# Optimization experiments

Hardware: AMD Instinct MI355X
Metric: run time of the kernel (lower is better)

## Reference

```python
import jax, jax.numpy as jnp
import numpy as np

B = 100000          # polymers
MOLS_PER = 4        # 3 monomers + 1 solvent per polymer
N = B * MOLS_PER
D = 64              # rdkit feature dim
F = 64              # polymer-level feature dim
H = 128             # hidden dim


def setup_inputs() -> dict:
    key = jax.random.key(0)
    ks = jax.random.split(key, 6)
    polymer_feats = jax.random.normal(ks[0], (B, F), dtype=jnp.float32)
    rdkit = jax.random.normal(ks[1], (N, D), dtype=jnp.float32)
    # sorted segment ids; last molecule of each segment is the solvent
    polymer_mapping = jnp.repeat(jnp.arange(B, dtype=jnp.int32), MOLS_PER)
    W1 = jax.random.normal(ks[2], (F + 2 * D, H), dtype=jnp.float32) * 0.05
    b1 = jnp.zeros((H,), jnp.float32)
    W2 = jax.random.normal(ks[3], (H, H // 2), dtype=jnp.float32) * 0.05
    b2 = jnp.zeros((H // 2,), jnp.float32)
    W3 = jax.random.normal(ks[4], (H // 2, 1), dtype=jnp.float32) * 0.05
    b3 = jnp.zeros((1,), jnp.float32)
    return {"polymer_feats": polymer_feats, "rdkit": rdkit,
            "polymer_mapping": polymer_mapping,
            "W1": W1, "b1": b1, "W2": W2, "b2": b2, "W3": W3, "b3": b3}


def _combine_rdkit(rdkit, polymer_mapping, num_polymers):
    # solvent = last row of each consecutive segment
    last = jnp.concatenate([polymer_mapping[1:] != polymer_mapping[:-1],
                            jnp.ones((1,), dtype=bool)])
    mono = ~last
    mono_w = mono.astype(rdkit.dtype)
    mono_sum = jax.ops.segment_sum(rdkit * mono_w[:, None], polymer_mapping,
                                   num_segments=num_polymers)
    mono_cnt = jax.ops.segment_sum(mono_w, polymer_mapping,
                                   num_segments=num_polymers)
    mono_avg = mono_sum / mono_cnt[:, None]
    solvent = jax.ops.segment_sum(rdkit * last.astype(rdkit.dtype)[:, None],
                                  polymer_mapping, num_segments=num_polymers)
    return jnp.concatenate([mono_avg, solvent], axis=1)  # [B, 2D]


def reference(polymer_feats, rdkit, polymer_mapping, W1, b1, W2, b2, W3, b3):
    num_polymers = polymer_feats.shape[0]
    pooled = _combine_rdkit(rdkit, polymer_mapping, num_polymers)
    x = jnp.concatenate([polymer_feats, pooled], axis=1)  # [B, F+2D]
    h = jax.nn.relu(x @ W1 + b1)          # dropout is identity in eval mode
    h = jax.nn.relu(h @ W2 + b2)
    return h @ W3 + b3                    # [B, 1]
```

## Files before the change

### kernel.cpp

```cpp
#include <hip/hip_runtime.h>

#define BPOLY  100000
#define TILE_M 64
#define NBLK   ((BPOLY + TILE_M - 1) / TILE_M)
#define KSTR   200

typedef __attribute__((ext_vector_type(8))) short          s16x8;
typedef __attribute__((ext_vector_type(4))) float          f32x4;
typedef __attribute__((ext_vector_type(4))) unsigned short u16x4;

__device__ __forceinline__ unsigned short f2bf(float x) {
  unsigned u = __float_as_uint(x);
  u += 0x7FFFu + ((u >> 16) & 1u);
  return (unsigned short)(u >> 16);
}
__device__ __forceinline__ float bf2f(unsigned short h) {
  return __uint_as_float(((unsigned)h) << 16);
}

#define W1H 0
#define W1L 24576
#define W2H 49152
#define W2L 57344

__global__ __launch_bounds__(256) void prep_weights(
    const float* __restrict__ W1,
    const float* __restrict__ W2,
    unsigned short* __restrict__ ws) {
  int i = blockIdx.x * 256 + threadIdx.x;
  if (i < 24576) {
    float v = W1[i];
    int k = i >> 7, n = i & 127;
    unsigned short h = f2bf(v);
    unsigned short l = f2bf(v - bf2f(h));
    ws[W1H + n * 192 + k] = h;
    ws[W1L + n * 192 + k] = l;
  } else {
    int j = i - 24576;
    float v = W2[j];
    int k = j >> 6, n = j & 63;
    unsigned short h = f2bf(v);
    unsigned short l = f2bf(v - bf2f(h));
    ws[W2H + n * 128 + k] = h;
    ws[W2L + n * 128 + k] = l;
  }
}

__global__ __launch_bounds__(256, 3) void fnn_mfma(
    const float* __restrict__ pf,
    const float* __restrict__ rdkit,
    const unsigned short* __restrict__ ws,
    const float* __restrict__ b1,
    const float* __restrict__ b2,
    const float* __restrict__ W3,
    const float* __restrict__ b3,
    float* __restrict__ out) {
  __shared__ __align__(16) unsigned short Xh[64 * KSTR];
  __shared__ __align__(16) unsigned short Xl[64 * KSTR];
  __shared__ float Psum[4 * 64];

  const int tid  = threadIdx.x;
  const int p0   = blockIdx.x * TILE_M;
  const int lane = tid & 63;
  const int wv   = tid >> 6;
  const int lmod = lane & 15;
  const int lq   = lane >> 4;

  #pragma unroll
  for (int i = 0; i < 4; ++i) {
    int f = tid + i * 256;
    int m = f >> 4, kq = (f & 15) * 4;
    float4 v = make_float4(0.f, 0.f, 0.f, 0.f);
    if (p0 + m < BPOLY) v = *(const float4*)(pf + (size_t)(p0 + m) * 64 + kq);
    float vv[4] = {v.x, v.y, v.z, v.w};
    u16x4 hh, hl;
    #pragma unroll
    for (int j = 0; j < 4; ++j) {
      unsigned short h = f2bf(vv[j]);
      hh[j] = h;
      hl[j] = f2bf(vv[j] - bf2f(h));
    }
    *(u16x4*)&Xh[m * KSTR + kq] = hh;
    *(u16x4*)&Xl[m * KSTR + kq] = hl;
  }
  #pragma unroll
  for (int i = 0; i < 4; ++i) {
    int f = tid + i * 256;
    int m = f >> 4, kq = (f & 15) * 4;
    float4 r0 = {0,0,0,0}, r1 = {0,0,0,0}, r2 = {0,0,0,0}, r3 = {0,0,0,0};
    if (p0 + m < BPOLY) {
      const float* base = rdkit + (size_t)(p0 + m) * 256 + kq;
      r0 = *(const float4*)(base);
      r1 = *(const float4*)(base + 64);
      r2 = *(const float4*)(base + 128);
      r3 = *(const float4*)(base + 192);
    }
    const float inv3 = 1.0f / 3.0f;
    float av[4] = {(r0.x + r1.x + r2.x) * inv3, (r0.y + r1.y + r2.y) * inv3,
                   (r0.z + r1.z + r2.z) * inv3, (r0.w + r1.w + r2.w) * inv3};
    float sv[4] = {r3.x, r3.y, r3.z, r3.w};
    u16x4 ahh, ahl, shh, shl;
    #pragma unroll
    for (int j = 0; j < 4; ++j) {
      unsigned short h = f2bf(av[j]);
      ahh[j] = h;  ahl[j] = f2bf(av[j] - bf2f(h));
      unsigned short s = f2bf(sv[j]);
      shh[j] = s;  shl[j] = f2bf(sv[j] - bf2f(s));
    }
    *(u16x4*)&Xh[m * KSTR + 64 + kq]  = ahh;
    *(u16x4*)&Xl[m * KSTR + 64 + kq]  = ahl;
    *(u16x4*)&Xh[m * KSTR + 128 + kq] = shh;
    *(u16x4*)&Xl[m * KSTR + 128 + kq] = shl;
  }
  __syncthreads();

  const float b1v0 = b1[32 * wv + lmod];
  const float b1v1 = b1[32 * wv + 16 + lmod];
  const unsigned short* w1h = ws + W1H;
  const unsigned short* w1l = ws + W1L;
  const int bcol0 = (32 * wv + lmod) * 192;
  const int bcol1 = (32 * wv + 16 + lmod) * 192;

  f32x4 acc1[4][2];
  #pragma unroll
  for (int mt = 0; mt < 4; ++mt) {
    acc1[mt][0] = (f32x4){0.f, 0.f, 0.f, 0.f};
    acc1[mt][1] = (f32x4){0.f, 0.f, 0.f, 0.f};
  }

  #pragma unroll 1
  for (int ks = 0; ks < 6; ++ks) {
    const int ko = ks * 32 + lq * 8;
    s16x8 bh0 = *(const s16x8*)(w1h + bcol0 + ko);
    s16x8 bl0 = *(const s16x8*)(w1l + bcol0 + ko);
    s16x8 bh1 = *(const s16x8*)(w1h + bcol1 + ko);
    s16x8 bl1 = *(const s16x8*)(w1l + bcol1 + ko);
    #pragma unroll
    for (int mt = 0; mt < 4; ++mt) {
      const int ra = (mt * 16 + lmod) * KSTR + ko;
      s16x8 ah = *(const s16x8*)&Xh[ra];
      s16x8 al = *(const s16x8*)&Xl[ra];
      acc1[mt][0] = __builtin_amdgcn_mfma_f32_16x16x32_bf16(ah, bh0, acc1[mt][0], 0, 0, 0);
      acc1[mt][0] = __builtin_amdgcn_mfma_f32_16x16x32_bf16(al, bh0, acc1[mt][0], 0, 0, 0);
      acc1[mt][0] = __builtin_amdgcn_mfma_f32_16x16x32_bf16(ah, bl0, acc1[mt][0], 0, 0, 0);
      acc1[mt][1] = __builtin_amdgcn_mfma_f32_16x16x32_bf16(ah, bh1, acc1[mt][1], 0, 0, 0);
      acc1[mt][1] = __builtin_amdgcn_mfma_f32_16x16x32_bf16(al, bh1, acc1[mt][1], 0, 0, 0);
      acc1[mt][1] = __builtin_amdgcn_mfma_f32_16x16x32_bf16(ah, bl1, acc1[mt][1], 0, 0, 0);
    }
  }

  __syncthreads();

  #pragma unroll
  for (int mt = 0; mt < 4; ++mt) {
    #pragma unroll
    for (int nn = 0; nn < 2; ++nn) {
      const float bv = nn ? b1v1 : b1v0;
      const int col = 32 * wv + 16 * nn + lmod;
      #pragma unroll
      for (int r = 0; r < 4; ++r) {
        float h = fmaxf(acc1[mt][nn][r] + bv, 0.f);
        unsigned short hh = f2bf(h);
        unsigned short hl = f2bf(h - bf2f(hh));
        const int row = mt * 16 + lq * 4 + r;
        Xh[row * KSTR + col] = hh;
        Xl[row * KSTR + col] = hl;
      }
    }
  }
  __syncthreads();

  const float b2v = b2[16 * wv + lmod];
  const float w3v = W3[16 * wv + lmod];
  const unsigned short* w2h = ws + W2H;
  const unsigned short* w2l = ws + W2L;
  const int bcol2 = (16 * wv + lmod) * 128;

  f32x4 acc2[4];
  #pragma unroll
  for (int mt = 0; mt < 4; ++mt) acc2[mt] = (f32x4){0.f, 0.f, 0.f, 0.f};

  #pragma unroll 1
  for (int ks = 0; ks < 4; ++ks) {
    const int ko = ks * 32 + lq * 8;
    s16x8 bh = *(const s16x8*)(w2h + bcol2 + ko);
    s16x8 bl = *(const s16x8*)(w2l + bcol2 + ko);
    #pragma unroll
    for (int mt = 0; mt < 4; ++mt) {
      const int ra = (mt * 16 + lmod) * KSTR + ko;
      s16x8 ah = *(const s16x8*)&Xh[ra];
      s16x8 al = *(const s16x8*)&Xl[ra];
      acc2[mt] = __builtin_amdgcn_mfma_f32_16x16x32_bf16(ah, bh, acc2[mt], 0, 0, 0);
      acc2[mt] = __builtin_amdgcn_mfma_f32_16x16x32_bf16(al, bh, acc2[mt], 0, 0, 0);
      acc2[mt] = __builtin_amdgcn_mfma_f32_16x16x32_bf16(ah, bl, acc2[mt], 0, 0, 0);
    }
  }

  float part[4][4];
  #pragma unroll
  for (int mt = 0; mt < 4; ++mt)
    #pragma unroll
    for (int r = 0; r < 4; ++r)
      part[mt][r] = fmaxf(acc2[mt][r] + b2v, 0.f) * w3v;

  #pragma unroll
  for (int mask = 1; mask <= 8; mask <<= 1)
    #pragma unroll
    for (int mt = 0; mt < 4; ++mt)
      #pragma unroll
      for (int r = 0; r < 4; ++r)
        part[mt][r] += __shfl_xor(part[mt][r], mask);

  if (lmod == 0) {
    #pragma unroll
    for (int mt = 0; mt < 4; ++mt)
      #pragma unroll
      for (int r = 0; r < 4; ++r)
        Psum[wv * 64 + mt * 16 + lq * 4 + r] = part[mt][r];
  }
  __syncthreads();

  if (tid < 64) {
    int p = p0 + tid;
    if (p < BPOLY)
      out[p] = Psum[tid] + Psum[64 + tid] + Psum[128 + tid] + Psum[192 + tid] + b3[0];
  }
}

extern "C" void kernel_launch(void* const* d_in, const int* in_sizes, int n_in,
                              void* d_out, int out_size, void* d_ws, size_t ws_size,
                              hipStream_t stream) {
  const float* pf    = (const float*)d_in[0];
  const float* rdkit = (const float*)d_in[1];
  const float* W1 = (const float*)d_in[3];
  const float* b1 = (const float*)d_in[4];
  const float* W2 = (const float*)d_in[5];
  const float* b2 = (const float*)d_in[6];
  const float* W3 = (const float*)d_in[7];
  const float* b3 = (const float*)d_in[8];
  unsigned short* ws = (unsigned short*)d_ws;
  float* out = (float*)d_out;

  prep_weights<<<128, 256, 0, stream>>>(W1, W2, ws);
  fnn_mfma<<<NBLK, 256, 0, stream>>>(pf, rdkit, ws, b1, b2, W3, b3, out);
}
```

Measured before the change: 213.5 us.

## Replace split-bf16 triple MFMA with single fp16 MFMA and halve LDS

Drops the hi/lo bf16 split emulation of fp32 (three MFMAs per tile) in favour of a single fp16 MFMA per tile, with fp16 activations and weights. This removes two thirds of the matrix work and the split-conversion ALU, and halves LDS use, which allows raising the occupancy hint to 6 blocks per CU. The partial-sum buffer is folded into the existing LDS tile and the K loops are unrolled by 2. The cost is reduced precision (fp16, 11-bit mantissa) and a risk of overflow for large values.

```diff
diff --git a/kernel.cpp b/kernel.cpp
--- a/kernel.cpp
+++ b/kernel.cpp
@@ -5,59 +5,38 @@
 #define NBLK   ((BPOLY + TILE_M - 1) / TILE_M)
 #define KSTR   200
 
-typedef __attribute__((ext_vector_type(8))) short          s16x8;
-typedef __attribute__((ext_vector_type(4))) float          f32x4;
-typedef __attribute__((ext_vector_type(4))) unsigned short u16x4;
+typedef __attribute__((ext_vector_type(8))) _Float16 f16x8;
+typedef __attribute__((ext_vector_type(4))) _Float16 f16x4;
+typedef __attribute__((ext_vector_type(4))) float    f32x4;
 
-__device__ __forceinline__ unsigned short f2bf(float x) {
-  unsigned u = __float_as_uint(x);
-  u += 0x7FFFu + ((u >> 16) & 1u);
-  return (unsigned short)(u >> 16);
-}
-__device__ __forceinline__ float bf2f(unsigned short h) {
-  return __uint_as_float(((unsigned)h) << 16);
-}
-
-#define W1H 0
-#define W1L 24576
-#define W2H 49152
-#define W2L 57344
+#define W1T 0
+#define W2T 24576
 
 __global__ __launch_bounds__(256) void prep_weights(
     const float* __restrict__ W1,
     const float* __restrict__ W2,
-    unsigned short* __restrict__ ws) {
+    _Float16* __restrict__ ws) {
   int i = blockIdx.x * 256 + threadIdx.x;
   if (i < 24576) {
-    float v = W1[i];
     int k = i >> 7, n = i & 127;
-    unsigned short h = f2bf(v);
-    unsigned short l = f2bf(v - bf2f(h));
-    ws[W1H + n * 192 + k] = h;
-    ws[W1L + n * 192 + k] = l;
+    ws[W1T + n * 192 + k] = (_Float16)W1[i];
   } else {
     int j = i - 24576;
-    float v = W2[j];
     int k = j >> 6, n = j & 63;
-    unsigned short h = f2bf(v);
-    unsigned short l = f2bf(v - bf2f(h));
-    ws[W2H + n * 128 + k] = h;
-    ws[W2L + n * 128 + k] = l;
+    ws[W2T + n * 128 + k] = (_Float16)W2[j];
   }
 }
 
-__global__ __launch_bounds__(256, 3) void fnn_mfma(
+__global__ __launch_bounds__(256, 6) void fnn_mfma(
     const float* __restrict__ pf,
     const float* __restrict__ rdkit,
-    const unsigned short* __restrict__ ws,
+    const _Float16* __restrict__ ws,
     const float* __restrict__ b1,
     const float* __restrict__ b2,
     const float* __restrict__ W3,
     const float* __restrict__ b3,
     float* __restrict__ out) {
-  __shared__ __align__(16) unsigned short Xh[64 * KSTR];
-  __shared__ __align__(16) unsigned short Xl[64 * KSTR];
-  __shared__ float Psum[4 * 64];
+  __shared__ __align__(16) _Float16 Xs[64 * KSTR];
 
   const int tid  = threadIdx.x;
   const int p0   = blockIdx.x * TILE_M;
@@ -72,16 +51,8 @@
     int m = f >> 4, kq = (f & 15) * 4;
     float4 v = make_float4(0.f, 0.f, 0.f, 0.f);
     if (p0 + m < BPOLY) v = *(const float4*)(pf + (size_t)(p0 + m) * 64 + kq);
-    float vv[4] = {v.x, v.y, v.z, v.w};
-    u16x4 hh, hl;
-    #pragma unroll
-    for (int j = 0; j < 4; ++j) {
-      unsigned short h = f2bf(vv[j]);
-      hh[j] = h;
-      hl[j] = f2bf(vv[j] - bf2f(h));
-    }
-    *(u16x4*)&Xh[m * KSTR + kq] = hh;
-    *(u16x4*)&Xl[m * KSTR + kq] = hl;
+    f16x4 h = {(_Float16)v.x, (_Float16)v.y, (_Float16)v.z, (_Float16)v.w};
+    *(f16x4*)&Xs[m * KSTR + kq] = h;
   }
   #pragma unroll
   for (int i = 0; i < 4; ++i) {
@@ -96,28 +67,19 @@
       r3 = *(const float4*)(base + 192);
     }
     const float inv3 = 1.0f / 3.0f;
-    float av[4] = {(r0.x + r1.x + r2.x) * inv3, (r0.y + r1.y + r2.y) * inv3,
-                   (r0.z + r1.z + r2.z) * inv3, (r0.w + r1.w + r2.w) * inv3};
-    float sv[4] = {r3.x, r3.y, r3.z, r3.w};
-    u16x4 ahh, ahl, shh, shl;
-    #pragma unroll
-    for (int j = 0; j < 4; ++j) {
-      unsigned short h = f2bf(av[j]);
-      ahh[j] = h;  ahl[j] = f2bf(av[j] - bf2f(h));
-      unsigned short s = f2bf(sv[j]);
-      shh[j] = s;  shl[j] = f2bf(sv[j] - bf2f(s));
-    }
-    *(u16x4*)&Xh[m * KSTR + 64 + kq]  = ahh;
-    *(u16x4*)&Xl[m * KSTR + 64 + kq]  = ahl;
-    *(u16x4*)&Xh[m * KSTR + 128 + kq] = shh;
-    *(u16x4*)&Xl[m * KSTR + 128 + kq] = shl;
+    f16x4 av = {(_Float16)((r0.x + r1.x + r2.x) * inv3),
+                (_Float16)((r0.y + r1.y + r2.y) * inv3),
+                (_Float16)((r0.z + r1.z + r2.z) * inv3),
+                (_Float16)((r0.w + r1.w + r2.w) * inv3)};
+    f16x4 sv = {(_Float16)r3.x, (_Float16)r3.y, (_Float16)r3.z, (_Float16)r3.w};
+    *(f16x4*)&Xs[m * KSTR + 64 + kq]  = av;
+    *(f16x4*)&Xs[m * KSTR + 128 + kq] = sv;
   }
   __syncthreads();
 
   const float b1v0 = b1[32 * wv + lmod];
   const float b1v1 = b1[32 * wv + 16 + lmod];
-  const unsigned short* w1h = ws + W1H;
-  const unsigned short* w1l = ws + W1L;
+  const _Float16* w1t = ws + W1T;
   const int bcol0 = (32 * wv + lmod) * 192;
   const int bcol1 = (32 * wv + 16 + lmod) * 192;
 
@@ -128,27 +90,18 @@
     acc1[mt][1] = (f32x4){0.f, 0.f, 0.f, 0.f};
   }
 
-  #pragma unroll 1
+  #pragma unroll 2
   for (int ks = 0; ks < 6; ++ks) {
     const int ko = ks * 32 + lq * 8;
-    s16x8 bh0 = *(const s16x8*)(w1h + bcol0 + ko);
-    s16x8 bl0 = *(const s16x8*)(w1l + bcol0 + ko);
-    s16x8 bh1 = *(const s16x8*)(w1h + bcol1 + ko);
-    s16x8 bl1 = *(const s16x8*)(w1l + bcol1 + ko);
+    f16x8 b0 = *(const f16x8*)(w1t + bcol0 + ko);
+    f16x8 b1f = *(const f16x8*)(w1t + bcol1 + ko);
     #pragma unroll
     for (int mt = 0; mt < 4; ++mt) {
-      const int ra = (mt * 16 + lmod) * KSTR + ko;
-      s16x8 ah = *(const s16x8*)&Xh[ra];
-      s16x8 al = *(const s16x8*)&Xl[ra];
-      acc1[mt][0] = __builtin_amdgcn_mfma_f32_16x16x32_bf16(ah, bh0, acc1[mt][0], 0, 0, 0);
-      acc1[mt][0] = __builtin_amdgcn_mfma_f32_16x16x32_bf16(al, bh0, acc1[mt][0], 0, 0, 0);
-      acc1[mt][0] = __builtin_amdgcn_mfma_f32_16x16x32_bf16(ah, bl0, acc1[mt][0], 0, 0, 0);
-      acc1[mt][1] = __builtin_amdgcn_mfma_f32_16x16x32_bf16(ah, bh1, acc1[mt][1], 0, 0, 0);
-      acc1[mt][1] = __builtin_amdgcn_mfma_f32_16x16x32_bf16(al, bh1, acc1[mt][1], 0, 0, 0);
-      acc1[mt][1] = __builtin_amdgcn_mfma_f32_16x16x32_bf16(ah, bl1, acc1[mt][1], 0, 0, 0);
+      f16x8 a = *(const f16x8*)&Xs[(mt * 16 + lmod) * KSTR + ko];
+      acc1[mt][0] = __builtin_amdgcn_mfma_f32_16x16x32_f16(a, b0,  acc1[mt][0], 0, 0, 0);
+      acc1[mt][1] = __builtin_amdgcn_mfma_f32_16x16x32_f16(a, b1f, acc1[mt][1], 0, 0, 0);
     }
   }
-
   __syncthreads();
 
   #pragma unroll
@@ -160,11 +113,7 @@
       #pragma unroll
       for (int r = 0; r < 4; ++r) {
         float h = fmaxf(acc1[mt][nn][r] + bv, 0.f);
-        unsigned short hh = f2bf(h);
-        unsigned short hl = f2bf(h - bf2f(hh));
-        const int row = mt * 16 + lq * 4 + r;
-        Xh[row * KSTR + col] = hh;
-        Xl[row * KSTR + col] = hl;
+        Xs[(mt * 16 + lq * 4 + r) * KSTR + col] = (_Float16)h;
       }
     }
   }
@@ -172,27 +121,21 @@
 
   const float b2v = b2[16 * wv + lmod];
   const float w3v = W3[16 * wv + lmod];
-  const unsigned short* w2h = ws + W2H;
-  const unsigned short* w2l = ws + W2L;
+  const _Float16* w2t = ws + W2T;
   const int bcol2 = (16 * wv + lmod) * 128;
 
   f32x4 acc2[4];
   #pragma unroll
   for (int mt = 0; mt < 4; ++mt) acc2[mt] = (f32x4){0.f, 0.f, 0.f, 0.f};
 
-  #pragma unroll 1
+  #pragma unroll 2
   for (int ks = 0; ks < 4; ++ks) {
     const int ko = ks * 32 + lq * 8;
-    s16x8 bh = *(const s16x8*)(w2h + bcol2 + ko);
-    s16x8 bl = *(const s16x8*)(w2l + bcol2 + ko);
+    f16x8 b = *(const f16x8*)(w2t + bcol2 + ko);
     #pragma unroll
     for (int mt = 0; mt < 4; ++mt) {
-      const int ra = (mt * 16 + lmod) * KSTR + ko;
-      s16x8 ah = *(const s16x8*)&Xh[ra];
-      s16x8 al = *(const s16x8*)&Xl[ra];
-      acc2[mt] = __builtin_amdgcn_mfma_f32_16x16x32_bf16(ah, bh, acc2[mt], 0, 0, 0);
-      acc2[mt] = __builtin_amdgcn_mfma_f32_16x16x32_bf16(al, bh, acc2[mt], 0, 0, 0);
-      acc2[mt] = __builtin_amdgcn_mfma_f32_16x16x32_bf16(ah, bl, acc2[mt], 0, 0, 0);
+      f16x8 a = *(const f16x8*)&Xs[(mt * 16 + lmod) * KSTR + ko];
+      acc2[mt] = __builtin_amdgcn_mfma_f32_16x16x32_f16(a, b, acc2[mt], 0, 0, 0);
     }
   }
 
@@ -215,15 +158,19 @@
     #pragma unroll
     for (int mt = 0; mt < 4; ++mt)
       #pragma unroll
-      for (int r = 0; r < 4; ++r)
-        Psum[wv * 64 + mt * 16 + lq * 4 + r] = part[mt][r];
+      for (int r = 0; r < 4; ++r) {
+        int row = mt * 16 + lq * 4 + r;
+        *(float*)&Xs[row * KSTR + 128 + 2 * wv] = part[mt][r];
+      }
   }
   __syncthreads();
 
   if (tid < 64) {
     int p = p0 + tid;
-    if (p < BPOLY)
-      out[p] = Psum[tid] + Psum[64 + tid] + Psum[128 + tid] + Psum[192 + tid] + b3[0];
+    if (p < BPOLY) {
+      float4 ps = *(const float4*)&Xs[tid * KSTR + 128];
+      out[p] = ps.x + ps.y + ps.z + ps.w + b3[0];
+    }
   }
 }
 
@@ -238,7 +185,7 @@
   const float* b2 = (const float*)d_in[6];
   const float* W3 = (const float*)d_in[7];
   const float* b3 = (const float*)d_in[8];
-  unsigned short* ws = (unsigned short*)d_ws;
+  _Float16* ws = (_Float16*)d_ws;
   float* out = (float*)d_out;
 
   prep_weights<<<128, 256, 0, stream>>>(W1, W2, ws);
```

New measurement: 195.4 us. 1.09x faster.
